# Performance work log

Hardware: AMD Instinct MI355X
Metric: run time of the kernel (lower is better)

## Reference

```python
import jax, jax.numpy as jnp
import numpy as np
import math

D_MODEL = 1024
N_HEADS = 16
D_HEAD = D_MODEL // N_HEADS
B, S = 4, 2048


def setup_inputs() -> dict:
    key = jax.random.key(0)
    ks = jax.random.split(key, 9)
    std = 1.0 / math.sqrt(D_MODEL)
    x = jax.random.normal(ks[0], (B, S, D_MODEL), dtype=jnp.float32)
    # causal mask: True = masked out
    mask = jnp.triu(jnp.ones((S, S), dtype=bool), k=1)
    Wq = jax.random.normal(ks[1], (D_MODEL, D_MODEL), jnp.float32) * std
    bq = jnp.zeros((D_MODEL,), jnp.float32)
    Wk = jax.random.normal(ks[2], (D_MODEL, D_MODEL), jnp.float32) * std
    bk = jnp.zeros((D_MODEL,), jnp.float32)
    Wv = jax.random.normal(ks[3], (D_MODEL, D_MODEL), jnp.float32) * std
    bv = jnp.zeros((D_MODEL,), jnp.float32)
    Wo = jax.random.normal(ks[4], (D_MODEL, D_MODEL), jnp.float32) * std
    bo = jnp.zeros((D_MODEL,), jnp.float32)
    return {"x": x, "mask": mask, "Wq": Wq, "bq": bq, "Wk": Wk, "bk": bk,
            "Wv": Wv, "bv": bv, "Wo": Wo, "bo": bo}


def reference(x, mask, Wq, bq, Wk, bk, Wv, bv, Wo, bo):
    b, s, _ = x.shape
    scale = math.sqrt(D_HEAD)
    # projections (Linear: x @ W.T + b), reshape to [b, h, s, d]
    def proj(W, bias):
        y = jnp.einsum('bsd,ed->bse', x, W) + bias
        return y.reshape(b, s, N_HEADS, D_HEAD).transpose(0, 2, 1, 3)
    q = proj(Wq, bq)
    k = proj(Wk, bk)
    v = proj(Wv, bv)
    scores = jnp.einsum('bhqd,bhkd->bhqk', q, k) / scale  # [b,h,s,s]
    scores = jnp.where(mask[None, None, :, :], -jnp.inf, scores)
    attn = jax.nn.softmax(scores, axis=-1)
    # dropout is identity in eval mode
    out = jnp.einsum('bhqk,bhkd->bhqd', attn, v)
    out = out.transpose(0, 2, 1, 3).reshape(b, s, D_MODEL)
    return jnp.einsum('bsd,ed->bse', out, Wo) + bo
```

## Files before the change

kernel.cpp:

```cpp
#include <hip/hip_runtime.h>
#include <stdint.h>

#define NH 16
#define DH 64
#define DM 1024
#define Bz 4
#define Sz 2048
#define NKT 16

typedef __bf16 bf16x8 __attribute__((ext_vector_type(8)));
typedef float f32x4 __attribute__((ext_vector_type(4)));

#define GLD_LDS16(gsrc, ldst)                                             \
    __builtin_amdgcn_global_load_lds(                                     \
        (const __attribute__((address_space(1))) void*)(gsrc),            \
        (__attribute__((address_space(3))) void*)(ldst), 16, 0, 0)

__device__ __forceinline__ unsigned short f2bf(float f) {
    unsigned u = __float_as_uint(f);
    u += 0x7FFFu + ((u >> 16) & 1u);
    return (unsigned short)(u >> 16);
}
__device__ __forceinline__ float bf2f(unsigned short h) {
    return __uint_as_float(((unsigned)h) << 16);
}

__global__ void detect_dtype(const unsigned short* __restrict__ xs,
                             int* __restrict__ flagp)
{
    const int t = threadIdx.x;
    int cnt = 0;
    for (int i = 0; i < 64; i++) {
        const unsigned short h = xs[(t * 64 + i) * 2];
        const int e = (h >> 7) & 0xFF;
        if (h != 0 && e >= 100 && e <= 130) cnt++;
    }
#pragma unroll
    for (int off = 32; off >= 1; off >>= 1)
        cnt += __shfl_xor(cnt, off);
    if (t == 0) *flagp = (cnt < 2048) ? 1 : 0;
}

__global__ __launch_bounds__(256) void convert_inputs(
    const void* s0, const void* s1, const void* s2, const void* s3,
    const void* s4, const void* s5, const void* s6, const void* s7,
    const void* s8,
    unsigned short* d0, unsigned short* d1, unsigned short* d2,
    unsigned short* d3, unsigned short* d4, unsigned short* d5,
    unsigned short* d6, unsigned short* d7, unsigned short* d8,
    const int* __restrict__ flagp)
{
    const void* s; unsigned short* d; int n;
    switch (blockIdx.y) {
        case 0: s = s0; d = d0; n = Bz * Sz * DM; break;
        case 1: s = s1; d = d1; n = DM * DM; break;
        case 2: s = s2; d = d2; n = DM * DM; break;
        case 3: s = s3; d = d3; n = DM * DM; break;
        case 4: s = s4; d = d4; n = DM * DM; break;
        case 5: s = s5; d = d5; n = DM; break;
        case 6: s = s6; d = d6; n = DM; break;
        case 7: s = s7; d = d7; n = DM; break;
        default: s = s8; d = d8; n = DM; break;
    }
    const int flag   = *flagp;
    const int stride = gridDim.x * blockDim.x * 4;
    const int base   = (blockIdx.x * blockDim.x + threadIdx.x) * 4;
    if (flag) {
        const float* sf = (const float*)s;
        for (int i = base; i < n; i += stride) {
            const float4 v = *reinterpret_cast<const float4*>(&sf[i]);
            ushort2 a, b;
            a.x = f2bf(v.x); a.y = f2bf(v.y);
            b.x = f2bf(v.z); b.y = f2bf(v.w);
            *reinterpret_cast<ushort2*>(&d[i])     = a;
            *reinterpret_cast<ushort2*>(&d[i + 2]) = b;
        }
    } else {
        const unsigned short* sh = (const unsigned short*)s;
        for (int i = base; i < n; i += stride)
            *reinterpret_cast<uint2*>(&d[i]) = *reinterpret_cast<const uint2*>(&sh[i]);
    }
}


__device__ __forceinline__ bf16x8 lds_frag(const unsigned short* lds, int R, int c) {
    const int cs = c ^ ((R & 7) << 4);
    return *reinterpret_cast<const bf16x8*>(
        reinterpret_cast<const char*>(lds) + R * 128 + cs);
}

__global__ __launch_bounds__(512, 2) void gemm_qkv(
    const unsigned short* __restrict__ X,
    const unsigned short* __restrict__ Wq,
    const unsigned short* __restrict__ Wk,
    const unsigned short* __restrict__ Wv,
    const unsigned short* __restrict__ bq,
    const unsigned short* __restrict__ bk,
    const unsigned short* __restrict__ bv,
    unsigned short* __restrict__ Qb,
    unsigned short* __restrict__ Kb,
    unsigned short* __restrict__ Vtb)
{
    __shared__ __align__(16) unsigned short Alds[2][256 * 64];
    __shared__ __align__(16) unsigned short Blds[2][256 * 64];

    const int tid  = threadIdx.x;
    const int w    = tid >> 6, lane = tid & 63;
    const int quad = lane >> 4, l15 = lane & 15;
    const int wr   = w >> 2, wc = w & 3;

    const int flat = (int)blockIdx.x;
    const int k8   = flat & 7;
    const int m    = flat >> 3;
    const int proj = m >> 4;
    const int mm   = m & 15;
    const int bm   = (k8 * 4 + (mm >> 2)) * 256;
    const int bn   = (mm & 3) * 256;

    const unsigned short* W      = proj == 0 ? Wq : (proj == 1 ? Wk : Wv);
    const unsigned short* bias_p = proj == 0 ? bq : (proj == 1 ? bk : bv);
    const unsigned short* Abase  = X + (size_t)bm * DM;
    const unsigned short* Bbase  = W + (size_t)bn * DM;

    const int srow = 8 * w + (lane >> 3);
    const int scb  = (lane & 7) * 16;
    const int ssc  = scb ^ ((srow & 7) << 4);

    f32x4 acc[8][4];
#pragma unroll
    for (int i = 0; i < 8; i++)
#pragma unroll
        for (int j = 0; j < 4; j++)
            acc[i][j] = f32x4{0.f, 0.f, 0.f, 0.f};

    auto stage_tile = [&](int buf, int kt) {
        const int kc = kt * 64;
#pragma unroll
        for (int q = 0; q < 2; q++) {
            const int r  = srow + 64 * q;
            const int ld = (64 * q + 8 * w) * 64;
            GLD_LDS16(&Abase[(size_t)(r      ) * DM + kc + (ssc >> 1)], &Alds[buf][ld]);
            GLD_LDS16(&Abase[(size_t)(r + 128) * DM + kc + (ssc >> 1)], &Alds[buf][ld + 128 * 64]);
            GLD_LDS16(&Bbase[(size_t)(r      ) * DM + kc + (ssc >> 1)], &Blds[buf][ld]);
            GLD_LDS16(&Bbase[(size_t)(r + 128) * DM + kc + (ssc >> 1)], &Blds[buf][ld + 128 * 64]);
        }
    };

    stage_tile(0, 0);
    asm volatile("s_waitcnt vmcnt(0)" ::: "memory");
    __builtin_amdgcn_s_barrier();
    asm volatile("" ::: "memory");

    for (int T = 0; T < NKT; ++T) {
        const int cur = T & 1;
        if (T < NKT - 1) stage_tile(cur ^ 1, T + 1);

        const unsigned short* A = &Alds[cur][0];
        const unsigned short* B = &Blds[cur][0];
        const int aR0 = wr * 128 + l15;
        const int bR0 = wc * 64 + l15;

        bf16x8 aR[4][2], b01[2][2], b23[2][2];
#pragma unroll
        for (int mi = 0; mi < 4; mi++) {
            aR[mi][0] = lds_frag(A, aR0 + mi * 16, quad * 16);
            aR[mi][1] = lds_frag(A, aR0 + mi * 16, quad * 16 + 64);
        }
#pragma unroll
        for (int nj = 0; nj < 2; nj++) {
            b01[nj][0] = lds_frag(B, bR0 + nj * 16, quad * 16);
            b01[nj][1] = lds_frag(B, bR0 + nj * 16, quad * 16 + 64);
        }
        __builtin_amdgcn_s_setprio(1);
#pragma unroll
        for (int mi = 0; mi < 4; mi++)
#pragma unroll
            for (int nj = 0; nj < 2; nj++) {
                acc[mi][nj] = __builtin_amdgcn_mfma_f32_16x16x32_bf16(aR[mi][0], b01[nj][0], acc[mi][nj], 0, 0, 0);
                acc[mi][nj] = __builtin_amdgcn_mfma_f32_16x16x32_bf16(aR[mi][1], b01[nj][1], acc[mi][nj], 0, 0, 0);
            }
        __builtin_amdgcn_s_setprio(0);
#pragma unroll
        for (int nj = 0; nj < 2; nj++) {
            b23[nj][0] = lds_frag(B, bR0 + (nj + 2) * 16, quad * 16);
            b23[nj][1] = lds_frag(B, bR0 + (nj + 2) * 16, quad * 16 + 64);
        }
        __builtin_amdgcn_s_setprio(1);
#pragma unroll
        for (int mi = 0; mi < 4; mi++)
#pragma unroll
            for (int nj = 0; nj < 2; nj++) {
                acc[mi][nj + 2] = __builtin_amdgcn_mfma_f32_16x16x32_bf16(aR[mi][0], b23[nj][0], acc[mi][nj + 2], 0, 0, 0);
                acc[mi][nj + 2] = __builtin_amdgcn_mfma_f32_16x16x32_bf16(aR[mi][1], b23[nj][1], acc[mi][nj + 2], 0, 0, 0);
            }
        __builtin_amdgcn_s_setprio(0);
#pragma unroll
        for (int mi = 0; mi < 4; mi++) {
            aR[mi][0] = lds_frag(A, aR0 + (mi + 4) * 16, quad * 16);
            aR[mi][1] = lds_frag(A, aR0 + (mi + 4) * 16, quad * 16 + 64);
        }
        __builtin_amdgcn_s_setprio(1);
#pragma unroll
        for (int mi = 0; mi < 4; mi++)
#pragma unroll
            for (int nj = 0; nj < 2; nj++) {
                acc[mi + 4][nj + 2] = __builtin_amdgcn_mfma_f32_16x16x32_bf16(aR[mi][0], b23[nj][0], acc[mi + 4][nj + 2], 0, 0, 0);
                acc[mi + 4][nj + 2] = __builtin_amdgcn_mfma_f32_16x16x32_bf16(aR[mi][1], b23[nj][1], acc[mi + 4][nj + 2], 0, 0, 0);
            }
#pragma unroll
        for (int mi = 0; mi < 4; mi++)
#pragma unroll
            for (int nj = 0; nj < 2; nj++) {
                acc[mi + 4][nj] = __builtin_amdgcn_mfma_f32_16x16x32_bf16(aR[mi][0], b01[nj][0], acc[mi + 4][nj], 0, 0, 0);
                acc[mi + 4][nj] = __builtin_amdgcn_mfma_f32_16x16x32_bf16(aR[mi][1], b01[nj][1], acc[mi + 4][nj], 0, 0, 0);
            }
        __builtin_amdgcn_s_setprio(0);

        asm volatile("s_waitcnt vmcnt(0)" ::: "memory");
        __builtin_amdgcn_s_barrier();
        asm volatile("" ::: "memory");
    }

    if (proj < 2) {
        unsigned short* dst = (proj == 0) ? Qb : Kb;
#pragma unroll
        for (int nj = 0; nj < 4; nj++) {
            const int   e    = bn + wc * 64 + nj * 16 + l15;
            const int   h    = e >> 6, dd = e & 63;
            const float bias = bf2f(bias_p[e]);
#pragma unroll
            for (int mi = 0; mi < 8; mi++) {
#pragma unroll
                for (int r = 0; r < 4; r++) {
                    const int mrow = bm + wr * 128 + mi * 16 + quad * 4 + r;
                    const int b = mrow >> 11, s = mrow & 2047;
                    dst[((size_t)(b * NH + h) * Sz + s) * DH + dd] = f2bf(acc[mi][nj][r] + bias);
                }
            }
        }
    } else {
#pragma unroll
        for (int nj = 0; nj < 4; nj++) {
            const int   e    = bn + wc * 64 + nj * 16 + l15;
            const int   h    = e >> 6, dd = e & 63;
            const float bias = bf2f(bias_p[e]);
#pragma unroll
            for (int mi = 0; mi < 8; mi++) {
                const int m0 = bm + wr * 128 + mi * 16 + quad * 4;
                const int b  = m0 >> 11, s0 = m0 & 2047;
                const unsigned u0 = __float_as_uint(acc[mi][nj][0] + bias) + 0x8000u;
                const unsigned u1 = __float_as_uint(acc[mi][nj][1] + bias) + 0x8000u;
                const unsigned u2 = __float_as_uint(acc[mi][nj][2] + bias) + 0x8000u;
                const unsigned u3 = __float_as_uint(acc[mi][nj][3] + bias) + 0x8000u;
                uint2 pk;
                pk.x = __builtin_amdgcn_perm(u1, u0, 0x07060302u);
                pk.y = __builtin_amdgcn_perm(u3, u2, 0x07060302u);
                *reinterpret_cast<uint2*>(
                    &Vtb[((size_t)(b * NH + h) * DH + dd) * Sz + s0]) = pk;
            }
        }
    }
}

__global__ __launch_bounds__(512) void flash_attn(
    const unsigned short* __restrict__ Qb,
    const unsigned short* __restrict__ Kb,
    const unsigned short* __restrict__ Vtb,
    unsigned short* __restrict__ AOb)
{
    __shared__ __align__(16) unsigned short Ks[64 * 72];
    __shared__ __align__(16) unsigned short Vs[64 * 72];
    __shared__ __align__(16) unsigned short Ps[128 * 72];

    const int tid  = threadIdx.x;
    const int w    = tid >> 6, lane = tid & 63;
    const int quad = lane >> 4, l15 = lane & 15;

    const int flat = (int)(blockIdx.y * gridDim.x + blockIdx.x);
    const int k8   = flat & 7;
    const int m    = flat >> 3;
    const int bh   = k8 + 8 * (m >> 3);
    const int cA   = m & 7;

    const int srow = tid >> 3;
    const int scc  = (tid & 7) * 8;
    const int hh = bh & 15, bb = bh >> 4;

    for (int pass = 0; pass < 2; pass++) {
        const int chunk = pass ? (15 - cA) : cA;
        const int qb = chunk * 128;
        const int qw = qb + w * 16;

        const size_t qbase = ((size_t)bh * Sz + qw + l15) * DH;
        const bf16x8 qf0 = *reinterpret_cast<const bf16x8*>(&Qb[qbase + quad * 8]);
        const bf16x8 qf1 = *reinterpret_cast<const bf16x8*>(&Qb[qbase + 32 + quad * 8]);

        f32x4 o[4];
#pragma unroll
        for (int jd = 0; jd < 4; jd++) o[jd] = f32x4{0.f, 0.f, 0.f, 0.f};
        float lsum = 0.f;

        const int n_kv = qb + 128;

        auto compute = [&](int kb) {
            const bool need_mask = (kb + 64 > qw);
#pragma unroll
            for (int j = 0; j < 4; j++) {
                const bf16x8 kf0 = *reinterpret_cast<const bf16x8*>(&Ks[(j * 16 + l15) * 72 + quad * 8]);
                const bf16x8 kf1 = *reinterpret_cast<const bf16x8*>(&Ks[(j * 16 + l15) * 72 + 32 + quad * 8]);
                f32x4 st = f32x4{0.f, 0.f, 0.f, 0.f};
                st = __builtin_amdgcn_mfma_f32_16x16x32_bf16(kf0, qf0, st, 0, 0, 0);
                st = __builtin_amdgcn_mfma_f32_16x16x32_bf16(kf1, qf1, st, 0, 0, 0);
                const int qa = qw + l15;
                float p[4];
#pragma unroll
                for (int r = 0; r < 4; r++) {
                    float e = __builtin_amdgcn_exp2f(st[r] * 0.18033688011f);
                    if (need_mask) {
                        const int kv = kb + j * 16 + quad * 4 + r;
                        e = (kv <= qa) ? e : 0.f;
                    }
                    p[r] = e;
                }
                lsum += (p[0] + p[1]) + (p[2] + p[3]);
                const unsigned u0 = __float_as_uint(p[0]) + 0x8000u;
                const unsigned u1 = __float_as_uint(p[1]) + 0x8000u;
                const unsigned u2 = __float_as_uint(p[2]) + 0x8000u;
                const unsigned u3 = __float_as_uint(p[3]) + 0x8000u;
                const unsigned pk0 = __builtin_amdgcn_perm(u1, u0, 0x07060302u);
                const unsigned pk1 = __builtin_amdgcn_perm(u3, u2, 0x07060302u);
                const int prow = (w * 16 + l15) * 72 + j * 16 + quad * 4;
                *reinterpret_cast<unsigned*>(&Ps[prow])     = pk0;
                *reinterpret_cast<unsigned*>(&Ps[prow + 2]) = pk1;
            }

            asm volatile("s_waitcnt lgkmcnt(0)" ::: "memory");

            const bf16x8 pf0 = *reinterpret_cast<const bf16x8*>(&Ps[(w * 16 + l15) * 72 + quad * 8]);
            const bf16x8 pf1 = *reinterpret_cast<const bf16x8*>(&Ps[(w * 16 + l15) * 72 + 32 + quad * 8]);
#pragma unroll
            for (int jd = 0; jd < 4; jd++) {
                const bf16x8 vf0 = *reinterpret_cast<const bf16x8*>(&Vs[(jd * 16 + l15) * 72 + quad * 8]);
                const bf16x8 vf1 = *reinterpret_cast<const bf16x8*>(&Vs[(jd * 16 + l15) * 72 + 32 + quad * 8]);
                o[jd] = __builtin_amdgcn_mfma_f32_16x16x32_bf16(pf0, vf0, o[jd], 0, 0, 0);
                o[jd] = __builtin_amdgcn_mfma_f32_16x16x32_bf16(pf1, vf1, o[jd], 0, 0, 0);
            }
        };

        uint4 kr0 = *reinterpret_cast<const uint4*>(&Kb[((size_t)bh * Sz + srow) * DH + scc]);
        uint4 vr0 = *reinterpret_cast<const uint4*>(&Vtb[((size_t)bh * DH + srow) * Sz + scc]);
        uint4 kr1, vr1;

        for (int kb = 0; kb < n_kv; kb += 128) {
            __syncthreads();
            *reinterpret_cast<uint4*>(&Ks[srow * 72 + scc]) = kr0;
            *reinterpret_cast<uint4*>(&Vs[srow * 72 + scc]) = vr0;
            kr1 = *reinterpret_cast<const uint4*>(&Kb[((size_t)bh * Sz + kb + 64 + srow) * DH + scc]);
            vr1 = *reinterpret_cast<const uint4*>(&Vtb[((size_t)bh * DH + srow) * Sz + kb + 64 + scc]);
            asm volatile("s_waitcnt lgkmcnt(0)" ::: "memory");
            __builtin_amdgcn_s_barrier();
            asm volatile("" ::: "memory");
            if (kb <= qw + 15) compute(kb);

            __syncthreads();
            *reinterpret_cast<uint4*>(&Ks[srow * 72 + scc]) = kr1;
            *reinterpret_cast<uint4*>(&Vs[srow * 72 + scc]) = vr1;
            if (kb + 128 < n_kv) {
                kr0 = *reinterpret_cast<const uint4*>(&Kb[((size_t)bh * Sz + kb + 128 + srow) * DH + scc]);
                vr0 = *reinterpret_cast<const uint4*>(&Vtb[((size_t)bh * DH + srow) * Sz + kb + 128 + scc]);
            }
            asm volatile("s_waitcnt lgkmcnt(0)" ::: "memory");
            __builtin_amdgcn_s_barrier();
            asm volatile("" ::: "memory");
            if (kb + 64 <= qw + 15) compute(kb + 64);
        }

        lsum += __shfl_xor(lsum, 16);
        lsum += __shfl_xor(lsum, 32);

        float linv[4];
#pragma unroll
        for (int r = 0; r < 4; r++)
            linv[r] = 1.0f / __shfl(lsum, quad * 4 + r);
#pragma unroll
        for (int jd = 0; jd < 4; jd++) {
#pragma unroll
            for (int r = 0; r < 4; r++) {
                const int s = qw + quad * 4 + r;
                AOb[((size_t)(bb * Sz + s)) * DM + hh * DH + jd * 16 + l15] =
                    f2bf(o[jd][r] * linv[r]);
            }
        }
    }
}

__global__ __launch_bounds__(512, 2) void gemm_out(
    const unsigned short* __restrict__ Ain,
    const unsigned short* __restrict__ W,
    const unsigned short* __restrict__ bo,
    void* __restrict__ outv,
    const int* __restrict__ flagp)
{
    __shared__ __align__(16) unsigned short Alds[2][256 * 64];
    __shared__ __align__(16) unsigned short Blds[2][256 * 64];

    const int tid  = threadIdx.x;
    const int w    = tid >> 6, lane = tid & 63;
    const int quad = lane >> 4, l15 = lane & 15;
    const int wr   = w >> 2, wc = w & 3;

    const int flat = (int)blockIdx.x;
    const int k8   = flat & 7;
    const int m    = flat >> 3;
    const int bm   = (k8 * 4 + (m >> 2)) * 256;
    const int bn   = (m & 3) * 256;

    const unsigned short* Abase = Ain + (size_t)bm * DM;
    const unsigned short* Bbase = W   + (size_t)bn * DM;

    const int srow = 8 * w + (lane >> 3);
    const int scb  = (lane & 7) * 16;
    const int ssc  = scb ^ ((srow & 7) << 4);

    f32x4 acc[8][4];
#pragma unroll
    for (int i = 0; i < 8; i++)
#pragma unroll
        for (int j = 0; j < 4; j++)
            acc[i][j] = f32x4{0.f, 0.f, 0.f, 0.f};

    auto stage_tile = [&](int buf, int kt) {
        const int kc = kt * 64;
#pragma unroll
        for (int q = 0; q < 2; q++) {
            const int r  = srow + 64 * q;
            const int ld = (64 * q + 8 * w) * 64;
            GLD_LDS16(&Abase[(size_t)(r      ) * DM + kc + (ssc >> 1)], &Alds[buf][ld]);
            GLD_LDS16(&Abase[(size_t)(r + 128) * DM + kc + (ssc >> 1)], &Alds[buf][ld + 128 * 64]);
            GLD_LDS16(&Bbase[(size_t)(r      ) * DM + kc + (ssc >> 1)], &Blds[buf][ld]);
            GLD_LDS16(&Bbase[(size_t)(r + 128) * DM + kc + (ssc >> 1)], &Blds[buf][ld + 128 * 64]);
        }
    };

    stage_tile(0, 0);
    asm volatile("s_waitcnt vmcnt(0)" ::: "memory");
    __builtin_amdgcn_s_barrier();
    asm volatile("" ::: "memory");

    for (int T = 0; T < NKT; ++T) {
        const int cur = T & 1;
        if (T < NKT - 1) stage_tile(cur ^ 1, T + 1);

        const unsigned short* A = &Alds[cur][0];
        const unsigned short* B = &Blds[cur][0];
        const int aR0 = wr * 128 + l15;
        const int bR0 = wc * 64 + l15;

        bf16x8 aR[4][2], b01[2][2], b23[2][2];
#pragma unroll
        for (int mi = 0; mi < 4; mi++) {
            aR[mi][0] = lds_frag(A, aR0 + mi * 16, quad * 16);
            aR[mi][1] = lds_frag(A, aR0 + mi * 16, quad * 16 + 64);
        }
#pragma unroll
        for (int nj = 0; nj < 2; nj++) {
            b01[nj][0] = lds_frag(B, bR0 + nj * 16, quad * 16);
            b01[nj][1] = lds_frag(B, bR0 + nj * 16, quad * 16 + 64);
        }
        __builtin_amdgcn_s_setprio(1);
#pragma unroll
        for (int mi = 0; mi < 4; mi++)
#pragma unroll
            for (int nj = 0; nj < 2; nj++) {
                acc[mi][nj] = __builtin_amdgcn_mfma_f32_16x16x32_bf16(aR[mi][0], b01[nj][0], acc[mi][nj], 0, 0, 0);
                acc[mi][nj] = __builtin_amdgcn_mfma_f32_16x16x32_bf16(aR[mi][1], b01[nj][1], acc[mi][nj], 0, 0, 0);
            }
        __builtin_amdgcn_s_setprio(0);
#pragma unroll
        for (int nj = 0; nj < 2; nj++) {
            b23[nj][0] = lds_frag(B, bR0 + (nj + 2) * 16, quad * 16);
            b23[nj][1] = lds_frag(B, bR0 + (nj + 2) * 16, quad * 16 + 64);
        }
        __builtin_amdgcn_s_setprio(1);
#pragma unroll
        for (int mi = 0; mi < 4; mi++)
#pragma unroll
            for (int nj = 0; nj < 2; nj++) {
                acc[mi][nj + 2] = __builtin_amdgcn_mfma_f32_16x16x32_bf16(aR[mi][0], b23[nj][0], acc[mi][nj + 2], 0, 0, 0);
                acc[mi][nj + 2] = __builtin_amdgcn_mfma_f32_16x16x32_bf16(aR[mi][1], b23[nj][1], acc[mi][nj + 2], 0, 0, 0);
            }
        __builtin_amdgcn_s_setprio(0);
#pragma unroll
        for (int mi = 0; mi < 4; mi++) {
            aR[mi][0] = lds_frag(A, aR0 + (mi + 4) * 16, quad * 16);
            aR[mi][1] = lds_frag(A, aR0 + (mi + 4) * 16, quad * 16 + 64);
        }
        __builtin_amdgcn_s_setprio(1);
#pragma unroll
        for (int mi = 0; mi < 4; mi++)
#pragma unroll
            for (int nj = 0; nj < 2; nj++) {
                acc[mi + 4][nj + 2] = __builtin_amdgcn_mfma_f32_16x16x32_bf16(aR[mi][0], b23[nj][0], acc[mi + 4][nj + 2], 0, 0, 0);
                acc[mi + 4][nj + 2] = __builtin_amdgcn_mfma_f32_16x16x32_bf16(aR[mi][1], b23[nj][1], acc[mi + 4][nj + 2], 0, 0, 0);
            }
#pragma unroll
        for (int mi = 0; mi < 4; mi++)
#pragma unroll
            for (int nj = 0; nj < 2; nj++) {
                acc[mi + 4][nj] = __builtin_amdgcn_mfma_f32_16x16x32_bf16(aR[mi][0], b01[nj][0], acc[mi + 4][nj], 0, 0, 0);
                acc[mi + 4][nj] = __builtin_amdgcn_mfma_f32_16x16x32_bf16(aR[mi][1], b01[nj][1], acc[mi + 4][nj], 0, 0, 0);
            }
        __builtin_amdgcn_s_setprio(0);

        asm volatile("s_waitcnt vmcnt(0)" ::: "memory");
        __builtin_amdgcn_s_barrier();
        asm volatile("" ::: "memory");
    }

    const int flag = *flagp;
    float*          outf = (float*)outv;
    unsigned short* outh = (unsigned short*)outv;
#pragma unroll
    for (int nj = 0; nj < 4; nj++) {
        const int   e    = bn + wc * 64 + nj * 16 + l15;
        const float bias = bf2f(bo[e]);
#pragma unroll
        for (int mi = 0; mi < 8; mi++) {
#pragma unroll
            for (int r = 0; r < 4; r++) {
                const int   mrow = bm + wr * 128 + mi * 16 + quad * 4 + r;
                const float v = acc[mi][nj][r] + bias;
                if (flag) outf[(size_t)mrow * DM + e] = v;
                else      outh[(size_t)mrow * DM + e] = f2bf(v);
            }
        }
    }
}

extern "C" void kernel_launch(void* const* d_in, const int* in_sizes, int n_in,
                              void* d_out, int out_size, void* d_ws, size_t ws_size,
                              hipStream_t stream) {
    const void* x = nullptr;
    const void* Wsrc[4] = {nullptr, nullptr, nullptr, nullptr};
    const void* bsrc[4] = {nullptr, nullptr, nullptr, nullptr};
    int nw = 0, nb = 0;
    for (int i = 0; i < n_in; i++) {
        const int sz = in_sizes[i];
        if (sz == Bz * Sz * DM)            { if (!x) x = d_in[i]; }
        else if (sz == DM * DM)            { if (nw < 4) Wsrc[nw++] = d_in[i]; }
        else if (sz == DM)                 { if (nb < 4) bsrc[nb++] = d_in[i]; }
    }

    char* wsb = (char*)d_ws;
    int*  flagp = (int*)wsb;
    unsigned short* Xc  = (unsigned short*)(wsb + 16);
    const size_t NX = (size_t)Bz * Sz * DM;
    const size_t NW = (size_t)DM * DM;
    unsigned short* Wc0 = Xc  + NX;
    unsigned short* Wc1 = Wc0 + NW;
    unsigned short* Wc2 = Wc1 + NW;
    unsigned short* Wc3 = Wc2 + NW;
    unsigned short* bc0 = Wc3 + NW;
    unsigned short* bc1 = bc0 + DM;
    unsigned short* bc2 = bc1 + DM;
    unsigned short* bc3 = bc2 + DM;
    unsigned short* Qb  = bc3 + DM;
    const size_t SZ = (size_t)Bz * NH * Sz * DH;
    unsigned short* Kb  = Qb  + SZ;
    unsigned short* Vtb = Kb  + SZ;
    unsigned short* AOb = Vtb + SZ;

    detect_dtype<<<1, 64, 0, stream>>>((const unsigned short*)x, flagp);
    convert_inputs<<<dim3(512, 9), 256, 0, stream>>>(
        x, Wsrc[0], Wsrc[1], Wsrc[2], Wsrc[3],
        bsrc[0], bsrc[1], bsrc[2], bsrc[3],
        Xc, Wc0, Wc1, Wc2, Wc3, bc0, bc1, bc2, bc3, flagp);

    gemm_qkv <<<dim3(384), 512, 0, stream>>>(Xc, Wc0, Wc1, Wc2, bc0, bc1, bc2, Qb, Kb, Vtb);
    flash_attn<<<dim3(8, 64), 512, 0, stream>>>(Qb, Kb, Vtb, AOb);
    gemm_out <<<dim3(128), 512, 0, stream>>>(AOb, Wc3, bc3, d_out, flagp);
}
```

Measured before the change: 316.4 us.

## Split GEMM tile staging into two halves with partial vmcnt waits; store Q/K row-major

Both GEMM kernels (QKV projection and output projection) now issue the next K-tile's global-to-LDS loads in two halves. The first half goes out before the first MFMA phase and the second after a mid-iteration barrier, with vmcnt(4) waits so one half can stay in flight while the other is consumed. The B-tile row mapping is reordered so that each half covers the rows consumed in the matching compute phase. Separately, Q and K are written in plain [B*S, DM] row-major order instead of a head-major scatter, and the attention kernel indexes them with a DM stride. The intent is finer-grained load/compute overlap and more contiguous projection stores, at the cost of an extra barrier per iteration and strided Q/K reads in attention.

```diff
diff --git a/kernel.cpp b/kernel.cpp
--- a/kernel.cpp
+++ b/kernel.cpp
@@ -124,7 +124,9 @@
 
     const int srow = 8 * w + (lane >> 3);
     const int scb  = (lane & 7) * 16;
-    const int ssc  = scb ^ ((srow & 7) << 4);
+    const int sse  = (scb ^ ((srow & 7) << 4)) >> 1;
+    const int br0  = (srow & 31) + ((srow >> 5) << 6);
+    const int bB   = 8 * w + ((w >= 4) ? 32 : 0);
 
     f32x4 acc[8][4];
 #pragma unroll
@@ -133,34 +135,37 @@
         for (int j = 0; j < 4; j++)
             acc[i][j] = f32x4{0.f, 0.f, 0.f, 0.f};
 
-    auto stage_tile = [&](int buf, int kt) {
+    auto stageH0 = [&](int buf, int kt) {
         const int kc = kt * 64;
-#pragma unroll
-        for (int q = 0; q < 2; q++) {
-            const int r  = srow + 64 * q;
-            const int ld = (64 * q + 8 * w) * 64;
-            GLD_LDS16(&Abase[(size_t)(r      ) * DM + kc + (ssc >> 1)], &Alds[buf][ld]);
-            GLD_LDS16(&Abase[(size_t)(r + 128) * DM + kc + (ssc >> 1)], &Alds[buf][ld + 128 * 64]);
-            GLD_LDS16(&Bbase[(size_t)(r      ) * DM + kc + (ssc >> 1)], &Blds[buf][ld]);
-            GLD_LDS16(&Bbase[(size_t)(r + 128) * DM + kc + (ssc >> 1)], &Blds[buf][ld + 128 * 64]);
-        }
+        GLD_LDS16(&Abase[(size_t)(srow      ) * DM + kc + sse], &Alds[buf][(8 * w      ) * 64]);
+        GLD_LDS16(&Abase[(size_t)(srow + 128) * DM + kc + sse], &Alds[buf][(8 * w + 128) * 64]);
+        GLD_LDS16(&Bbase[(size_t)(br0       ) * DM + kc + sse], &Blds[buf][(bB         ) * 64]);
+        GLD_LDS16(&Bbase[(size_t)(br0  + 128) * DM + kc + sse], &Blds[buf][(bB    + 128) * 64]);
     };
-
-    stage_tile(0, 0);
-    asm volatile("s_waitcnt vmcnt(0)" ::: "memory");
+    auto stageH1 = [&](int buf, int kt) {
+        const int kc = kt * 64;
+        GLD_LDS16(&Abase[(size_t)(srow +  64) * DM + kc + sse], &Alds[buf][(8 * w +  64) * 64]);
+        GLD_LDS16(&Abase[(size_t)(srow + 192) * DM + kc + sse], &Alds[buf][(8 * w + 192) * 64]);
+        GLD_LDS16(&Bbase[(size_t)(br0  +  32) * DM + kc + sse], &Blds[buf][(bB    +  32) * 64]);
+        GLD_LDS16(&Bbase[(size_t)(br0  + 160) * DM + kc + sse], &Blds[buf][(bB    + 160) * 64]);
+    };
+
+    stageH0(0, 0);
+    stageH1(0, 0);
+    asm volatile("s_waitcnt vmcnt(4)" ::: "memory");
     __builtin_amdgcn_s_barrier();
     asm volatile("" ::: "memory");
 
     for (int T = 0; T < NKT; ++T) {
-        const int cur = T & 1;
-        if (T < NKT - 1) stage_tile(cur ^ 1, T + 1);
-
+        const int cur = T & 1, nxt = cur ^ 1;
         const unsigned short* A = &Alds[cur][0];
         const unsigned short* B = &Blds[cur][0];
         const int aR0 = wr * 128 + l15;
         const int bR0 = wc * 64 + l15;
 
         bf16x8 aR[4][2], b01[2][2], b23[2][2];
+
+        if (T < NKT - 1) stageH0(nxt, T + 1);
 #pragma unroll
         for (int mi = 0; mi < 4; mi++) {
             aR[mi][0] = lds_frag(A, aR0 + mi * 16, quad * 16);
@@ -180,6 +185,12 @@
                 acc[mi][nj] = __builtin_amdgcn_mfma_f32_16x16x32_bf16(aR[mi][1], b01[nj][1], acc[mi][nj], 0, 0, 0);
             }
         __builtin_amdgcn_s_setprio(0);
+        if (T < NKT - 1) { asm volatile("s_waitcnt vmcnt(4)" ::: "memory"); }
+        else             { asm volatile("s_waitcnt vmcnt(0)" ::: "memory"); }
+        __builtin_amdgcn_s_barrier();
+        asm volatile("" ::: "memory");
+
+        if (T < NKT - 1) stageH1(nxt, T + 1);
 #pragma unroll
         for (int nj = 0; nj < 2; nj++) {
             b23[nj][0] = lds_frag(B, bR0 + (nj + 2) * 16, quad * 16);
@@ -194,6 +205,7 @@
                 acc[mi][nj + 2] = __builtin_amdgcn_mfma_f32_16x16x32_bf16(aR[mi][1], b23[nj][1], acc[mi][nj + 2], 0, 0, 0);
             }
         __builtin_amdgcn_s_setprio(0);
+
 #pragma unroll
         for (int mi = 0; mi < 4; mi++) {
             aR[mi][0] = lds_frag(A, aR0 + (mi + 4) * 16, quad * 16);
@@ -216,7 +228,8 @@
             }
         __builtin_amdgcn_s_setprio(0);
 
-        asm volatile("s_waitcnt vmcnt(0)" ::: "memory");
+        if (T < NKT - 1) { asm volatile("s_waitcnt vmcnt(4)" ::: "memory"); }
+        else             { asm volatile("s_waitcnt vmcnt(0)" ::: "memory"); }
         __builtin_amdgcn_s_barrier();
         asm volatile("" ::: "memory");
     }
@@ -226,15 +239,13 @@
 #pragma unroll
         for (int nj = 0; nj < 4; nj++) {
             const int   e    = bn + wc * 64 + nj * 16 + l15;
-            const int   h    = e >> 6, dd = e & 63;
             const float bias = bf2f(bias_p[e]);
 #pragma unroll
             for (int mi = 0; mi < 8; mi++) {
 #pragma unroll
                 for (int r = 0; r < 4; r++) {
                     const int mrow = bm + wr * 128 + mi * 16 + quad * 4 + r;
-                    const int b = mrow >> 11, s = mrow & 2047;
-                    dst[((size_t)(b * NH + h) * Sz + s) * DH + dd] = f2bf(acc[mi][nj][r] + bias);
+                    dst[(size_t)mrow * DM + e] = f2bf(acc[mi][nj][r] + bias);
                 }
             }
         }
@@ -291,7 +302,7 @@
         const int qb = chunk * 128;
         const int qw = qb + w * 16;
 
-        const size_t qbase = ((size_t)bh * Sz + qw + l15) * DH;
+        const size_t qbase = ((size_t)(bb * Sz + qw + l15)) * DM + hh * DH;
         const bf16x8 qf0 = *reinterpret_cast<const bf16x8*>(&Qb[qbase + quad * 8]);
         const bf16x8 qf1 = *reinterpret_cast<const bf16x8*>(&Qb[qbase + 32 + quad * 8]);
 
@@ -347,7 +358,7 @@
             }
         };
 
-        uint4 kr0 = *reinterpret_cast<const uint4*>(&Kb[((size_t)bh * Sz + srow) * DH + scc]);
+        uint4 kr0 = *reinterpret_cast<const uint4*>(&Kb[((size_t)(bb * Sz + srow)) * DM + hh * DH + scc]);
         uint4 vr0 = *reinterpret_cast<const uint4*>(&Vtb[((size_t)bh * DH + srow) * Sz + scc]);
         uint4 kr1, vr1;
 
@@ -355,7 +366,7 @@
             __syncthreads();
             *reinterpret_cast<uint4*>(&Ks[srow * 72 + scc]) = kr0;
             *reinterpret_cast<uint4*>(&Vs[srow * 72 + scc]) = vr0;
-            kr1 = *reinterpret_cast<const uint4*>(&Kb[((size_t)bh * Sz + kb + 64 + srow) * DH + scc]);
+            kr1 = *reinterpret_cast<const uint4*>(&Kb[((size_t)(bb * Sz + kb + 64 + srow)) * DM + hh * DH + scc]);
             vr1 = *reinterpret_cast<const uint4*>(&Vtb[((size_t)bh * DH + srow) * Sz + kb + 64 + scc]);
             asm volatile("s_waitcnt lgkmcnt(0)" ::: "memory");
             __builtin_amdgcn_s_barrier();
@@ -366,7 +377,7 @@
             *reinterpret_cast<uint4*>(&Ks[srow * 72 + scc]) = kr1;
             *reinterpret_cast<uint4*>(&Vs[srow * 72 + scc]) = vr1;
             if (kb + 128 < n_kv) {
-                kr0 = *reinterpret_cast<const uint4*>(&Kb[((size_t)bh * Sz + kb + 128 + srow) * DH + scc]);
+                kr0 = *reinterpret_cast<const uint4*>(&Kb[((size_t)(bb * Sz + kb + 128 + srow)) * DM + hh * DH + scc]);
                 vr0 = *reinterpret_cast<const uint4*>(&Vtb[((size_t)bh * DH + srow) * Sz + kb + 128 + scc]);
             }
             asm volatile("s_waitcnt lgkmcnt(0)" ::: "memory");
@@ -420,7 +431,9 @@
 
     const int srow = 8 * w + (lane >> 3);
     const int scb  = (lane & 7) * 16;
-    const int ssc  = scb ^ ((srow & 7) << 4);
+    const int sse  = (scb ^ ((srow & 7) << 4)) >> 1;
+    const int br0  = (srow & 31) + ((srow >> 5) << 6);
+    const int bB   = 8 * w + ((w >= 4) ? 32 : 0);
 
     f32x4 acc[8][4];
 #pragma unroll
@@ -429,34 +442,37 @@
         for (int j = 0; j < 4; j++)
             acc[i][j] = f32x4{0.f, 0.f, 0.f, 0.f};
 
-    auto stage_tile = [&](int buf, int kt) {
+    auto stageH0 = [&](int buf, int kt) {
         const int kc = kt * 64;
-#pragma unroll
-        for (int q = 0; q < 2; q++) {
-            const int r  = srow + 64 * q;
-            const int ld = (64 * q + 8 * w) * 64;
-            GLD_LDS16(&Abase[(size_t)(r      ) * DM + kc + (ssc >> 1)], &Alds[buf][ld]);
-            GLD_LDS16(&Abase[(size_t)(r + 128) * DM + kc + (ssc >> 1)], &Alds[buf][ld + 128 * 64]);
-            GLD_LDS16(&Bbase[(size_t)(r      ) * DM + kc + (ssc >> 1)], &Blds[buf][ld]);
-            GLD_LDS16(&Bbase[(size_t)(r + 128) * DM + kc + (ssc >> 1)], &Blds[buf][ld + 128 * 64]);
-        }
+        GLD_LDS16(&Abase[(size_t)(srow      ) * DM + kc + sse], &Alds[buf][(8 * w      ) * 64]);
+        GLD_LDS16(&Abase[(size_t)(srow + 128) * DM + kc + sse], &Alds[buf][(8 * w + 128) * 64]);
+        GLD_LDS16(&Bbase[(size_t)(br0       ) * DM + kc + sse], &Blds[buf][(bB         ) * 64]);
+        GLD_LDS16(&Bbase[(size_t)(br0  + 128) * DM + kc + sse], &Blds[buf][(bB    + 128) * 64]);
     };
-
-    stage_tile(0, 0);
-    asm volatile("s_waitcnt vmcnt(0)" ::: "memory");
+    auto stageH1 = [&](int buf, int kt) {
+        const int kc = kt * 64;
+        GLD_LDS16(&Abase[(size_t)(srow +  64) * DM + kc + sse], &Alds[buf][(8 * w +  64) * 64]);
+        GLD_LDS16(&Abase[(size_t)(srow + 192) * DM + kc + sse], &Alds[buf][(8 * w + 192) * 64]);
+        GLD_LDS16(&Bbase[(size_t)(br0  +  32) * DM + kc + sse], &Blds[buf][(bB    +  32) * 64]);
+        GLD_LDS16(&Bbase[(size_t)(br0  + 160) * DM + kc + sse], &Blds[buf][(bB    + 160) * 64]);
+    };
+
+    stageH0(0, 0);
+    stageH1(0, 0);
+    asm volatile("s_waitcnt vmcnt(4)" ::: "memory");
     __builtin_amdgcn_s_barrier();
     asm volatile("" ::: "memory");
 
     for (int T = 0; T < NKT; ++T) {
-        const int cur = T & 1;
-        if (T < NKT - 1) stage_tile(cur ^ 1, T + 1);
-
+        const int cur = T & 1, nxt = cur ^ 1;
         const unsigned short* A = &Alds[cur][0];
         const unsigned short* B = &Blds[cur][0];
         const int aR0 = wr * 128 + l15;
         const int bR0 = wc * 64 + l15;
 
         bf16x8 aR[4][2], b01[2][2], b23[2][2];
+
+        if (T < NKT - 1) stageH0(nxt, T + 1);
 #pragma unroll
         for (int mi = 0; mi < 4; mi++) {
             aR[mi][0] = lds_frag(A, aR0 + mi * 16, quad * 16);
@@ -476,6 +492,12 @@
                 acc[mi][nj] = __builtin_amdgcn_mfma_f32_16x16x32_bf16(aR[mi][1], b01[nj][1], acc[mi][nj], 0, 0, 0);
             }
         __builtin_amdgcn_s_setprio(0);
+        if (T < NKT - 1) { asm volatile("s_waitcnt vmcnt(4)" ::: "memory"); }
+        else             { asm volatile("s_waitcnt vmcnt(0)" ::: "memory"); }
+        __builtin_amdgcn_s_barrier();
+        asm volatile("" ::: "memory");
+
+        if (T < NKT - 1) stageH1(nxt, T + 1);
 #pragma unroll
         for (int nj = 0; nj < 2; nj++) {
             b23[nj][0] = lds_frag(B, bR0 + (nj + 2) * 16, quad * 16);
@@ -490,6 +512,7 @@
                 acc[mi][nj + 2] = __builtin_amdgcn_mfma_f32_16x16x32_bf16(aR[mi][1], b23[nj][1], acc[mi][nj + 2], 0, 0, 0);
             }
         __builtin_amdgcn_s_setprio(0);
+
 #pragma unroll
         for (int mi = 0; mi < 4; mi++) {
             aR[mi][0] = lds_frag(A, aR0 + (mi + 4) * 16, quad * 16);
@@ -512,7 +535,8 @@
             }
         __builtin_amdgcn_s_setprio(0);
 
-        asm volatile("s_waitcnt vmcnt(0)" ::: "memory");
+        if (T < NKT - 1) { asm volatile("s_waitcnt vmcnt(4)" ::: "memory"); }
+        else             { asm volatile("s_waitcnt vmcnt(0)" ::: "memory"); }
         __builtin_amdgcn_s_barrier();
         asm volatile("" ::: "memory");
     }
```

Result: slower. 330.9 us (+4.6%).
